# Kernel tuning notes

Measured on AMD Instinct MI355X. Metric: run time of the kernel, lower is better.

## Reference

```python
import jax, jax.numpy as jnp
import numpy as np
from jax import lax

B, N, NIN, NOUT, K = 8, 4096, 64, 128, 32
RATIO, R = 0.25, 0.15
M = int(N * RATIO)
DIM = NIN + 4       # x_j concat 4 point-pair features


def setup_inputs() -> dict:
    key = jax.random.key(0)
    ks = jax.random.split(key, 10)
    x = jax.random.normal(ks[0], (B, N, NIN), jnp.float32)
    pos = jax.random.uniform(ks[1], (B, N, 3), jnp.float32)
    nrm = jax.random.normal(ks[2], (B, N, 3), jnp.float32)
    norm = nrm / jnp.linalg.norm(nrm, axis=-1, keepdims=True)
    batch = jnp.broadcast_to(jnp.arange(B, dtype=jnp.int32)[:, None], (B, N))
    s = 0.05
    W1 = jax.random.normal(ks[3], (DIM, DIM), jnp.float32) * s
    b1 = jnp.zeros((DIM,), jnp.float32)
    W2 = jax.random.normal(ks[4], (DIM, DIM), jnp.float32) * s
    b2 = jnp.zeros((DIM,), jnp.float32)
    W3 = jax.random.normal(ks[5], (DIM, NOUT), jnp.float32) * s
    b3 = jnp.zeros((NOUT,), jnp.float32)
    return dict(x=x, pos=pos, norm=norm, batch=batch,
                W1=W1, b1=b1, W2=W2, b2=b2, W3=W3, b3=b3)


def fps(pos):
    """Farthest point sampling, deterministic start at index 0. pos: [N,3] -> [M] int32."""
    n = pos.shape[0]
    def step(carry, _):
        dists, last = carry
        d = jnp.sum((pos - pos[last]) ** 2, axis=-1)
        dists = jnp.minimum(dists, d)
        nxt = jnp.argmax(dists).astype(jnp.int32)
        return (dists, nxt), last
    init = (jnp.full((n,), jnp.inf, pos.dtype), jnp.int32(0))
    (_, _), idx = lax.scan(step, init, None, length=M)
    return idx


def _angle(v1, v2):
    c = jnp.cross(v1, v2)
    return jnp.arctan2(jnp.linalg.norm(c, axis=-1), jnp.sum(v1 * v2, axis=-1))


def reference(x, pos, norm, batch, W1, b1, W2, b2, W3, b3):
    # batch is implicit in the leading B dim (equal-size clouds); arg kept for parity.
    idx = jax.vmap(fps)(pos)                                   # [B,M]
    pos_s = jnp.take_along_axis(pos, idx[..., None], axis=1)   # [B,M,3]
    norm_s = jnp.take_along_axis(norm, idx[..., None], axis=1) # [B,M,3]

    # radius neighbor search: K nearest within R per sampled center
    d2 = jnp.sum((pos_s[:, :, None, :] - pos[:, None, :, :]) ** 2, axis=-1)  # [B,M,N]
    masked = jnp.where(d2 <= R * R, d2, jnp.inf)
    negv, nbr = lax.top_k(-masked, K)                          # [B,M,K]
    valid = jnp.isfinite(negv)                                 # self always valid (d2=0)

    gather = jax.vmap(lambda a, i: a[i])                       # per-batch fancy gather
    x_j = gather(x, nbr)        # [B,M,K,NIN]
    pos_j = gather(pos, nbr)    # [B,M,K,3]
    norm_j = gather(norm, nbr)  # [B,M,K,3]

    d = pos_j - pos_s[:, :, None, :]                           # pos_j - pos_i
    n_i = jnp.broadcast_to(norm_s[:, :, None, :], norm_j.shape)
    ppf = jnp.stack([
        jnp.linalg.norm(d, axis=-1),
        _angle(n_i, d),
        _angle(norm_j, d),
        _angle(n_i, norm_j),
    ], axis=-1)                                                # [B,M,K,4]

    msg = jnp.concatenate([x_j, ppf], axis=-1)                 # [B,M,K,DIM]
    h = jax.nn.relu(msg @ W1 + b1)
    h = jax.nn.relu(h @ W2 + b2)
    h = jnp.where(valid[..., None], h, -jnp.inf)
    agg = jnp.max(h, axis=2)                                   # max aggregation [B,M,DIM]
    out = jax.nn.relu(agg @ W3 + b3)                           # global_nn [B,M,NOUT]
    return out, pos_s, idx
```

## Files before the change

### kernel.cpp

```cpp
#include <hip/hip_runtime.h>
#include <hip/hip_bf16.h>
#include <math.h>

#define BB 8
#define NN 4096
#define NIN 64
#define NOUTF 128
#define KNB 32
#define MM 1024
#define DIM 68
#define CAP 320

typedef float f32x2 __attribute__((ext_vector_type(2)));

__device__ __forceinline__ f32x2 pk_add(f32x2 a, f32x2 b)
{
    f32x2 d;
    asm("v_pk_add_f32 %0, %1, %2" : "=v"(d) : "v"(a), "v"(b));
    return d;
}
__device__ __forceinline__ f32x2 pk_mul(f32x2 a, f32x2 b)
{
    f32x2 d;
    asm("v_pk_mul_f32 %0, %1, %2" : "=v"(d) : "v"(a), "v"(b));
    return d;
}

__device__ __forceinline__ f32x2 pkmax(f32x2 a, f32x2 b)
{
    f32x2 r; r.x = fmaxf(a.x, b.x); r.y = fmaxf(a.y, b.y); return r;
}

template <int CTRL>
__device__ __forceinline__ float dppmax(float v)
{
    int m = __builtin_amdgcn_update_dpp(__float_as_int(v), __float_as_int(v),
                                        CTRL, 0xF, 0xF, false);
    return fmaxf(v, __int_as_float(m));
}

__global__ __launch_bounds__(256) void fps_kernel(
    const float* __restrict__ pos,
    int* __restrict__ idx_ws,
    float* __restrict__ out_pos_s, float* __restrict__ out_idx)
{
#pragma clang fp contract(off)
    __shared__ float4 posL[NN];
    __shared__ f32x2  slot[2][4];
    __shared__ float4 emitP[MM];
    __shared__ int    emitI[MM];

    const int b    = blockIdx.x;
    const int tid  = threadIdx.x;
    const int wv   = tid >> 6;
    const int lane = tid & 63;
    const float* pb = pos + (size_t)b * NN * 3;

    f32x2 X[8], Y[8], Z[8], D[8];
#pragma unroll
    for (int j = 0; j < 8; ++j) {
        int pA = tid * 16 + 2 * j;
        X[j].x = pb[pA * 3 + 0]; X[j].y = pb[pA * 3 + 3];
        Y[j].x = pb[pA * 3 + 1]; Y[j].y = pb[pA * 3 + 4];
        Z[j].x = pb[pA * 3 + 2]; Z[j].y = pb[pA * 3 + 5];
        D[j].x = INFINITY;       D[j].y = INFINITY;
    }
#pragma unroll
    for (int j = 0; j < 16; ++j) {
        int p2 = tid + 256 * j;
        posL[p2] = make_float4(pb[p2 * 3 + 0], pb[p2 * 3 + 1],
                               pb[p2 * 3 + 2], 0.0f);
    }
    __syncthreads();

    int   last = 0;
    float lx = pb[0], ly = pb[1], lz = pb[2];

#pragma unroll 2
    for (int t = 0; t < MM; ++t) {
        if (tid == 0) {
            emitP[t] = make_float4(lx, ly, lz, 0.0f);
            emitI[t] = last;
        }

        float nx = -lx, ny = -ly, nz = -lz;
        f32x2 nx2; nx2.x = nx; nx2.y = nx;
        f32x2 ny2; ny2.x = ny; ny2.y = ny;
        f32x2 nz2; nz2.x = nz; nz2.y = nz;

#pragma unroll
        for (int j = 0; j < 8; ++j) {
            f32x2 dx = pk_add(X[j], nx2);
            f32x2 dy = pk_add(Y[j], ny2);
            f32x2 dz = pk_add(Z[j], nz2);
            f32x2 xx = pk_mul(dx, dx);
            f32x2 yy = pk_mul(dy, dy);
            f32x2 zz = pk_mul(dz, dz);
            f32x2 s  = pk_add(pk_add(xx, yy), zz);
            D[j].x = fminf(D[j].x, s.x);
            D[j].y = fminf(D[j].y, s.y);
        }
        f32x2 m0 = pkmax(pkmax(D[0], D[1]), pkmax(D[2], D[3]));
        f32x2 m1 = pkmax(pkmax(D[4], D[5]), pkmax(D[6], D[7]));
        f32x2 mm = pkmax(m0, m1);
        float bv = fmaxf(mm.x, mm.y);

        int k0 = (D[0].x == bv) ? 0  : ((D[0].y == bv) ? 1  : 16);
        int k1 = (D[1].x == bv) ? 2  : ((D[1].y == bv) ? 3  : 16);
        int k2 = (D[2].x == bv) ? 4  : ((D[2].y == bv) ? 5  : 16);
        int k3 = (D[3].x == bv) ? 6  : ((D[3].y == bv) ? 7  : 16);
        int k4 = (D[4].x == bv) ? 8  : ((D[4].y == bv) ? 9  : 16);
        int k5 = (D[5].x == bv) ? 10 : ((D[5].y == bv) ? 11 : 16);
        int k6 = (D[6].x == bv) ? 12 : ((D[6].y == bv) ? 13 : 16);
        int k7 = (D[7].x == bv) ? 14 : ((D[7].y == bv) ? 15 : 16);
        k0 = min(k0, k4); k1 = min(k1, k5); k2 = min(k2, k6); k3 = min(k3, k7);
        k0 = min(k0, k2); k1 = min(k1, k3);
        int kmin = min(k0, k1);
        int p_cand = tid * 16 + kmin;

        float r = bv;
        r = dppmax<0x111>(r);
        r = dppmax<0x112>(r);
        r = dppmax<0x114>(r);
        r = dppmax<0x118>(r);
        r = dppmax<0x142>(r);
        r = dppmax<0x143>(r);
        float wmax = __int_as_float(__builtin_amdgcn_readlane(__float_as_int(r), 63));

        unsigned long long msk = __ballot(bv == wmax);
        int wl = __ffsll((long long)msk) - 1;
        int pwin_wave = __builtin_amdgcn_readlane(p_cand, wl);

        const int p_ = t & 1;
        if (lane == 0) {
            f32x2 sv; sv.x = wmax; sv.y = __int_as_float(pwin_wave);
            slot[p_][wv] = sv;
        }
        __syncthreads();

        f32x2 s0 = slot[p_][0], s1 = slot[p_][1];
        f32x2 s2 = slot[p_][2], s3 = slot[p_][3];
        float cv = s0.x; int ci = __float_as_int(s0.y);
        {
            int i1 = __float_as_int(s1.y);
            bool bt = (s1.x > cv) || (s1.x == cv && i1 < ci);
            cv = bt ? s1.x : cv; ci = bt ? i1 : ci;
        }
        {
            int i2 = __float_as_int(s2.y);
            bool bt = (s2.x > cv) || (s2.x == cv && i2 < ci);
            cv = bt ? s2.x : cv; ci = bt ? i2 : ci;
        }
        {
            int i3 = __float_as_int(s3.y);
            bool bt = (s3.x > cv) || (s3.x == cv && i3 < ci);
            cv = bt ? s3.x : cv; ci = bt ? i3 : ci;
        }

        float4 cw = posL[ci];
        last = ci; lx = cw.x; ly = cw.y; lz = cw.z;
    }

    __syncthreads();
    for (int u = tid; u < MM; u += 256) {
        float4 rec = emitP[u];
        int    id  = emitI[u];
        int base = b * MM + u;
        idx_ws[base]  = id;
        out_idx[base] = (float)id;
        out_pos_s[base * 3 + 0] = rec.x;
        out_pos_s[base * 3 + 1] = rec.y;
        out_pos_s[base * 3 + 2] = rec.z;
    }
}

__global__ __launch_bounds__(256) void radius_kernel(
    const float* __restrict__ pos,
    const float* __restrict__ pos_s,
    int* __restrict__ nbr_ws, int* __restrict__ nvalid_ws)
{
    __shared__ float d2L[4][CAP];
    __shared__ int   idL[4][CAP];
    __shared__ int   cntL[4];

    const int wv = threadIdx.x >> 6, lane = threadIdx.x & 63;
    const int c = blockIdx.x * 4 + wv;
    const int b = c >> 10;
    const float RSQ = 0.0225f;

    if (lane == 0) cntL[wv] = 0;

    float cx = pos_s[c * 3 + 0];
    float cy = pos_s[c * 3 + 1];
    float cz = pos_s[c * 3 + 2];
    const float* pb = pos + (size_t)b * NN * 3;

    for (int it = 0; it < NN / 64; ++it) {
        int p = it * 64 + lane;
        float dx = __fsub_rn(cx, pb[p * 3 + 0]);
        float dy = __fsub_rn(cy, pb[p * 3 + 1]);
        float dz = __fsub_rn(cz, pb[p * 3 + 2]);
        float d2 = __fadd_rn(__fadd_rn(__fmul_rn(dx, dx), __fmul_rn(dy, dy)),
                             __fmul_rn(dz, dz));
        if (d2 <= RSQ) {
            int slot = atomicAdd(&cntL[wv], 1);
            if (slot < CAP) { d2L[wv][slot] = d2; idL[wv][slot] = p; }
        }
    }
    int n = cntL[wv];
    if (n > CAP) n = CAP;

    if (n <= KNB) {
        if (lane == 0) nvalid_ws[c] = n;
        if (lane < n) nbr_ws[c * KNB + lane] = idL[wv][lane];
    } else {
        if (lane == 0) nvalid_ws[c] = KNB;
        for (int a = lane; a < n; a += 64) {
            float da = d2L[wv][a]; int ia = idL[wv][a];
            int r = 0;
            for (int jj = 0; jj < n; ++jj) {
                float dj = d2L[wv][jj]; int ij = idL[wv][jj];
                r += (dj < da || (dj == da && ij < ia)) ? 1 : 0;
            }
            if (r < KNB) nbr_ws[c * KNB + r] = ia;
        }
    }
}

__device__ __forceinline__ float angle3(float ax, float ay, float az,
                                        float bx, float by, float bz)
{
    float cx = ay * bz - az * by;
    float cy = az * bx - ax * bz;
    float cz = ax * by - ay * bx;
    float cn = sqrtf(cx * cx + cy * cy + cz * cz);
    float dt = ax * bx + ay * by + az * bz;
    return atan2f(cn, dt);
}

__device__ __forceinline__ float4 fma4(float m, float4 w, float4 a)
{
    a.x = fmaf(m, w.x, a.x);
    a.y = fmaf(m, w.y, a.y);
    a.z = fmaf(m, w.z, a.z);
    a.w = fmaf(m, w.w, a.w);
    return a;
}

__device__ __forceinline__ void layer_pass(const float* __restrict__ inL,
                                           const float* __restrict__ Ws,
                                           const float* __restrict__ bs,
                                           float* __restrict__ outL, int t)
{
    const int e = t & 63, wvi = t >> 6;
    const bool has5 = (wvi == 0);
    const int j0 = wvi * 4, j1 = (wvi + 4) * 4, j2 = (wvi + 8) * 4,
              j3 = (wvi + 12) * 4, j4 = 64;

    float4 a0 = *reinterpret_cast<const float4*>(bs + j0);
    float4 a1 = *reinterpret_cast<const float4*>(bs + j1);
    float4 a2 = *reinterpret_cast<const float4*>(bs + j2);
    float4 a3 = *reinterpret_cast<const float4*>(bs + j3);
    float4 a4 = has5 ? *reinterpret_cast<const float4*>(bs + j4)
                     : make_float4(0.f, 0.f, 0.f, 0.f);

    const float* row = inL + e * 69;
#pragma unroll 4
    for (int i = 0; i < DIM; ++i) {
        float m = row[i];
        const float* wr = Ws + i * DIM;
        a0 = fma4(m, *reinterpret_cast<const float4*>(wr + j0), a0);
        a1 = fma4(m, *reinterpret_cast<const float4*>(wr + j1), a1);
        a2 = fma4(m, *reinterpret_cast<const float4*>(wr + j2), a2);
        a3 = fma4(m, *reinterpret_cast<const float4*>(wr + j3), a3);
        if (has5) a4 = fma4(m, *reinterpret_cast<const float4*>(wr + j4), a4);
    }

    float* orow = outL + e * 69;
    orow[j0 + 0] = fmaxf(a0.x, 0.f); orow[j0 + 1] = fmaxf(a0.y, 0.f);
    orow[j0 + 2] = fmaxf(a0.z, 0.f); orow[j0 + 3] = fmaxf(a0.w, 0.f);
    orow[j1 + 0] = fmaxf(a1.x, 0.f); orow[j1 + 1] = fmaxf(a1.y, 0.f);
    orow[j1 + 2] = fmaxf(a1.z, 0.f); orow[j1 + 3] = fmaxf(a1.w, 0.f);
    orow[j2 + 0] = fmaxf(a2.x, 0.f); orow[j2 + 1] = fmaxf(a2.y, 0.f);
    orow[j2 + 2] = fmaxf(a2.z, 0.f); orow[j2 + 3] = fmaxf(a2.w, 0.f);
    orow[j3 + 0] = fmaxf(a3.x, 0.f); orow[j3 + 1] = fmaxf(a3.y, 0.f);
    orow[j3 + 2] = fmaxf(a3.z, 0.f); orow[j3 + 3] = fmaxf(a3.w, 0.f);
    if (has5) {
        orow[64] = fmaxf(a4.x, 0.f); orow[65] = fmaxf(a4.y, 0.f);
        orow[66] = fmaxf(a4.z, 0.f); orow[67] = fmaxf(a4.w, 0.f);
    }
}

__global__ __launch_bounds__(256) void mlp_kernel(
    const float* __restrict__ x, const float* __restrict__ pos,
    const float* __restrict__ norm,
    const float* __restrict__ W1, const float* __restrict__ b1,
    const float* __restrict__ W2, const float* __restrict__ b2,
    const float* __restrict__ W3, const float* __restrict__ b3,
    const int* __restrict__ idx_ws, const float* __restrict__ pos_s,
    const int* __restrict__ nbr_ws, const int* __restrict__ nvalid_ws,
    float* __restrict__ out)
{
    __shared__ alignas(16) float W1s[DIM * DIM];
    __shared__ alignas(16) float W2s[DIM * DIM];
    __shared__ alignas(16) float b1s[DIM];
    __shared__ alignas(16) float b2s[DIM];
    __shared__ float msgL[64 * 69];
    __shared__ float h1L[64 * 69];
    __shared__ float aggL[2 * DIM];
    __shared__ int   nvL[2], jLs[64];

    const int t = threadIdx.x;
    const int cg0 = blockIdx.x * 2;

    for (int u = t; u < DIM * DIM; u += 256) { W1s[u] = W1[u]; W2s[u] = W2[u]; }
    if (t < DIM) { b1s[t] = b1[t]; b2s[t] = b2[t]; }
    if (t < 2) nvL[t] = min(nvalid_ws[cg0 + t], KNB);
    __syncthreads();

    const int e = t & 63, fc = t >> 6;
    const int lc = e >> 5, slot = e & 31;
    const int c = cg0 + lc;
    const int b = c >> 10;

    if (fc == 0) {
        int nv = nvL[lc];
        jLs[e] = (slot < nv) ? nbr_ws[c * KNB + slot] : 0;
    }
    __syncthreads();

    const int j = jLs[e];
    {
        const float* xj = x + ((size_t)b * NN + j) * NIN + fc * 16;
#pragma unroll
        for (int r = 0; r < 4; ++r) {
            float4 v = *reinterpret_cast<const float4*>(xj + r * 4);
            msgL[e * 69 + fc * 16 + r * 4 + 0] = v.x;
            msgL[e * 69 + fc * 16 + r * 4 + 1] = v.y;
            msgL[e * 69 + fc * 16 + r * 4 + 2] = v.z;
            msgL[e * 69 + fc * 16 + r * 4 + 3] = v.w;
        }
    }
    if (fc == 0) {
        float pix = pos_s[c * 3 + 0];
        float piy = pos_s[c * 3 + 1];
        float piz = pos_s[c * 3 + 2];
        int ic = idx_ws[c];
        const float* pj_ = pos  + ((size_t)b * NN + j) * 3;
        const float* nj_ = norm + ((size_t)b * NN + j) * 3;
        const float* ni_ = norm + ((size_t)b * NN + ic) * 3;
        float dx = pj_[0] - pix, dy = pj_[1] - piy, dz = pj_[2] - piz;
        float nix = ni_[0], niy = ni_[1], niz = ni_[2];
        float njx = nj_[0], njy = nj_[1], njz = nj_[2];
        msgL[e * 69 + 64] = sqrtf(dx * dx + dy * dy + dz * dz);
        msgL[e * 69 + 65] = angle3(nix, niy, niz, dx, dy, dz);
        msgL[e * 69 + 66] = angle3(njx, njy, njz, dx, dy, dz);
        msgL[e * 69 + 67] = angle3(nix, niy, niz, njx, njy, njz);
    }
    __syncthreads();

    layer_pass(msgL, W1s, b1s, h1L, t);
    __syncthreads();
    layer_pass(h1L, W2s, b2s, msgL, t);
    __syncthreads();

    if (t < 2 * DIM) {
        int cc = t / DIM, jf = t % DIM;
        int nv = nvL[cc];
        float v = -INFINITY;
        for (int s = 0; s < nv; ++s)
            v = fmaxf(v, msgL[(cc * 32 + s) * 69 + jf]);
        aggL[cc * DIM + jf] = v;
    }
    __syncthreads();

    {
        int cc = t >> 7, o = t & 127;
        int cgl = cg0 + cc;
        float acc = b3[o];
#pragma unroll 4
        for (int i = 0; i < DIM; ++i)
            acc = fmaf(aggL[cc * DIM + i], W3[i * NOUTF + o], acc);
        out[(size_t)cgl * NOUTF + o] = fmaxf(acc, 0.0f);
    }
}

extern "C" void kernel_launch(void* const* d_in, const int* in_sizes, int n_in,
                              void* d_out, int out_size, void* d_ws, size_t ws_size,
                              hipStream_t stream)
{
    const float* x    = (const float*)d_in[0];
    const float* pos  = (const float*)d_in[1];
    const float* norm = (const float*)d_in[2];
    const float* W1 = (const float*)d_in[4];
    const float* b1 = (const float*)d_in[5];
    const float* W2 = (const float*)d_in[6];
    const float* b2 = (const float*)d_in[7];
    const float* W3 = (const float*)d_in[8];
    const float* b3 = (const float*)d_in[9];

    float* out       = (float*)d_out;
    float* out_pos_s = out + (size_t)BB * MM * NOUTF;
    float* out_idx   = out_pos_s + (size_t)BB * MM * 3;

    char* ws = (char*)d_ws;
    int*   idx_ws    = (int*)ws;
    int*   nbr_ws    = (int*)(ws + 131072);
    int*   nvalid_ws = (int*)(ws + 131072 + (size_t)BB * MM * KNB * 4);

    fps_kernel<<<dim3(BB), dim3(256), 0, stream>>>(pos, idx_ws,
                                                   out_pos_s, out_idx);
    radius_kernel<<<dim3((BB * MM) / 4), dim3(256), 0, stream>>>(pos, out_pos_s,
                                                                 nbr_ws, nvalid_ws);
    mlp_kernel<<<dim3((BB * MM) / 2), dim3(256), 0, stream>>>(
        x, pos, norm, W1, b1, W2, b2, W3, b3,
        idx_ws, out_pos_s, nbr_ws, nvalid_ws, out);
}
```

Measured before the change: 956.8 us.

## Fuse radius neighbor search into the MLP kernel

Removes the separate radius_kernel and runs the ball query inside the MLP kernel. Each half of the block (128 threads) scans the cloud for one center and keeps neighbors in shared memory. This drops one launch and the global round trip of the neighbor index and count arrays. In exchange, shared memory per block grows and the scan now uses 128 lanes per center instead of 64, which may reduce occupancy of the MLP phase.

```diff
diff --git a/kernel.cpp b/kernel.cpp
--- a/kernel.cpp
+++ b/kernel.cpp
@@ -174,59 +174,6 @@
     }
 }
 
-__global__ __launch_bounds__(256) void radius_kernel(
-    const float* __restrict__ pos,
-    const float* __restrict__ pos_s,
-    int* __restrict__ nbr_ws, int* __restrict__ nvalid_ws)
-{
-    __shared__ float d2L[4][CAP];
-    __shared__ int   idL[4][CAP];
-    __shared__ int   cntL[4];
-
-    const int wv = threadIdx.x >> 6, lane = threadIdx.x & 63;
-    const int c = blockIdx.x * 4 + wv;
-    const int b = c >> 10;
-    const float RSQ = 0.0225f;
-
-    if (lane == 0) cntL[wv] = 0;
-
-    float cx = pos_s[c * 3 + 0];
-    float cy = pos_s[c * 3 + 1];
-    float cz = pos_s[c * 3 + 2];
-    const float* pb = pos + (size_t)b * NN * 3;
-
-    for (int it = 0; it < NN / 64; ++it) {
-        int p = it * 64 + lane;
-        float dx = __fsub_rn(cx, pb[p * 3 + 0]);
-        float dy = __fsub_rn(cy, pb[p * 3 + 1]);
-        float dz = __fsub_rn(cz, pb[p * 3 + 2]);
-        float d2 = __fadd_rn(__fadd_rn(__fmul_rn(dx, dx), __fmul_rn(dy, dy)),
-                             __fmul_rn(dz, dz));
-        if (d2 <= RSQ) {
-            int slot = atomicAdd(&cntL[wv], 1);
-            if (slot < CAP) { d2L[wv][slot] = d2; idL[wv][slot] = p; }
-        }
-    }
-    int n = cntL[wv];
-    if (n > CAP) n = CAP;
-
-    if (n <= KNB) {
-        if (lane == 0) nvalid_ws[c] = n;
-        if (lane < n) nbr_ws[c * KNB + lane] = idL[wv][lane];
-    } else {
-        if (lane == 0) nvalid_ws[c] = KNB;
-        for (int a = lane; a < n; a += 64) {
-            float da = d2L[wv][a]; int ia = idL[wv][a];
-            int r = 0;
-            for (int jj = 0; jj < n; ++jj) {
-                float dj = d2L[wv][jj]; int ij = idL[wv][jj];
-                r += (dj < da || (dj == da && ij < ia)) ? 1 : 0;
-            }
-            if (r < KNB) nbr_ws[c * KNB + r] = ia;
-        }
-    }
-}
-
 __device__ __forceinline__ float angle3(float ax, float ay, float az,
                                         float bx, float by, float bz)
 {
@@ -291,14 +238,13 @@
     }
 }
 
-__global__ __launch_bounds__(256) void mlp_kernel(
+__global__ __launch_bounds__(256) void fused_kernel(
     const float* __restrict__ x, const float* __restrict__ pos,
     const float* __restrict__ norm,
     const float* __restrict__ W1, const float* __restrict__ b1,
     const float* __restrict__ W2, const float* __restrict__ b2,
     const float* __restrict__ W3, const float* __restrict__ b3,
     const int* __restrict__ idx_ws, const float* __restrict__ pos_s,
-    const int* __restrict__ nbr_ws, const int* __restrict__ nvalid_ws,
     float* __restrict__ out)
 {
     __shared__ alignas(16) float W1s[DIM * DIM];
@@ -308,14 +254,64 @@
     __shared__ float msgL[64 * 69];
     __shared__ float h1L[64 * 69];
     __shared__ float aggL[2 * DIM];
-    __shared__ int   nvL[2], jLs[64];
+    __shared__ float d2L[2][CAP];
+    __shared__ int   idL[2][CAP];
+    __shared__ int   cntL[2];
+    __shared__ int   nbrL[2][KNB];
+    __shared__ int   nvL[2];
 
     const int t = threadIdx.x;
     const int cg0 = blockIdx.x * 2;
 
     for (int u = t; u < DIM * DIM; u += 256) { W1s[u] = W1[u]; W2s[u] = W2[u]; }
     if (t < DIM) { b1s[t] = b1[t]; b2s[t] = b2[t]; }
-    if (t < 2) nvL[t] = min(nvalid_ws[cg0 + t], KNB);
+    if (t < 2) cntL[t] = 0;
+    __syncthreads();
+
+    {
+        const int half  = t >> 7;
+        const int hlane = t & 127;
+        const int c  = cg0 + half;
+        const int bb = c >> 10;
+        const float RSQ = 0.0225f;
+
+        float cx = pos_s[c * 3 + 0];
+        float cy = pos_s[c * 3 + 1];
+        float cz = pos_s[c * 3 + 2];
+        const float* pb = pos + (size_t)bb * NN * 3;
+
+        for (int it = 0; it < NN / 128; ++it) {
+            int p = it * 128 + hlane;
+            float dx = __fsub_rn(cx, pb[p * 3 + 0]);
+            float dy = __fsub_rn(cy, pb[p * 3 + 1]);
+            float dz = __fsub_rn(cz, pb[p * 3 + 2]);
+            float d2 = __fadd_rn(__fadd_rn(__fmul_rn(dx, dx), __fmul_rn(dy, dy)),
+                                 __fmul_rn(dz, dz));
+            if (d2 <= RSQ) {
+                int s = atomicAdd(&cntL[half], 1);
+                if (s < CAP) { d2L[half][s] = d2; idL[half][s] = p; }
+            }
+        }
+        __syncthreads();
+
+        int n = cntL[half];
+        if (n > CAP) n = CAP;
+        if (hlane == 0) nvL[half] = min(n, KNB);
+
+        if (n <= KNB) {
+            if (hlane < n) nbrL[half][hlane] = idL[half][hlane];
+        } else {
+            for (int a = hlane; a < n; a += 128) {
+                float da = d2L[half][a]; int ia = idL[half][a];
+                int r = 0;
+                for (int jj = 0; jj < n; ++jj) {
+                    float dj = d2L[half][jj]; int ij = idL[half][jj];
+                    r += (dj < da || (dj == da && ij < ia)) ? 1 : 0;
+                }
+                if (r < KNB) nbrL[half][r] = ia;
+            }
+        }
+    }
     __syncthreads();
 
     const int e = t & 63, fc = t >> 6;
@@ -323,13 +319,9 @@
     const int c = cg0 + lc;
     const int b = c >> 10;
 
-    if (fc == 0) {
-        int nv = nvL[lc];
-        jLs[e] = (slot < nv) ? nbr_ws[c * KNB + slot] : 0;
-    }
-    __syncthreads();
-
-    const int j = jLs[e];
+    const int nv = nvL[lc];
+    const int j  = (slot < nv) ? nbrL[lc][slot] : 0;
+
     {
         const float* xj = x + ((size_t)b * NN + j) * NIN + fc * 16;
 #pragma unroll
@@ -366,9 +358,9 @@
 
     if (t < 2 * DIM) {
         int cc = t / DIM, jf = t % DIM;
-        int nv = nvL[cc];
+        int nvv = nvL[cc];
         float v = -INFINITY;
-        for (int s = 0; s < nv; ++s)
+        for (int s = 0; s < nvv; ++s)
             v = fmaxf(v, msgL[(cc * 32 + s) * 69 + jf]);
         aggL[cc * DIM + jf] = v;
     }
@@ -404,15 +396,11 @@
     float* out_idx   = out_pos_s + (size_t)BB * MM * 3;
 
     char* ws = (char*)d_ws;
-    int*   idx_ws    = (int*)ws;
-    int*   nbr_ws    = (int*)(ws + 131072);
-    int*   nvalid_ws = (int*)(ws + 131072 + (size_t)BB * MM * KNB * 4);
+    int* idx_ws = (int*)ws;
 
     fps_kernel<<<dim3(BB), dim3(256), 0, stream>>>(pos, idx_ws,
                                                    out_pos_s, out_idx);
-    radius_kernel<<<dim3((BB * MM) / 4), dim3(256), 0, stream>>>(pos, out_pos_s,
-                                                                 nbr_ws, nvalid_ws);
-    mlp_kernel<<<dim3((BB * MM) / 2), dim3(256), 0, stream>>>(
+    fused_kernel<<<dim3((BB * MM) / 2), dim3(256), 0, stream>>>(
         x, pos, norm, W1, b1, W2, b2, W3, b3,
-        idx_ws, out_pos_s, nbr_ws, nvalid_ws, out);
-}
+        idx_ws, out_pos_s, out);
+}
```

Measured after the change: 1.021 ms. 6.7% more time.
